# Optimization experiments

Hardware: AMD Instinct MI355X
Metric: run time of the kernel (lower is better)

The kernel has to match this reference:

```python
import jax, jax.numpy as jnp
import numpy as np

B, C, H, W = 8, 64, 64, 64
CI = 32  # inter_channels = in_channels // 2
EPS = 1e-5


def conv1x1(x, w, b=None):
    # x: (b,c,h,w), w: (o,c) -> (b,o,h,w)
    y = jnp.einsum('bchw,oc->bohw', x, w)
    if b is not None:
        y = y + b[None, :, None, None]
    return y


def maxpool2x2(x):
    b, c, h, w = x.shape
    return x.reshape(b, c, h // 2, 2, w // 2, 2).max(axis=(3, 5))


def setup_inputs() -> dict:
    key = jax.random.key(0)
    ks = jax.random.split(key, 12)
    s = 0.05
    return {
        'x': jax.random.normal(ks[0], (B, C, H, W), jnp.float32),
        'theta_w': jax.random.normal(ks[1], (CI, C), jnp.float32) * s,
        'theta_b': jax.random.normal(ks[2], (CI,), jnp.float32) * s,
        'phi_w': jax.random.normal(ks[3], (CI, C), jnp.float32) * s,
        'phi_b': jax.random.normal(ks[4], (CI,), jnp.float32) * s,
        'psi_w': jax.random.normal(ks[5], (CI, C), jnp.float32) * s,
        'psi_b': jax.random.normal(ks[6], (CI,), jnp.float32) * s,
        'cp_w': jax.random.normal(ks[7], (2 * CI,), jnp.float32) * s,  # concat_project 1x1, no bias
        'W_w': jax.random.normal(ks[8], (C, CI + 1), jnp.float32) * s,
        'W_b': jax.random.normal(ks[9], (C,), jnp.float32) * s,
        'bn_gamma': jax.random.normal(ks[10], (C,), jnp.float32) * s + 1.0,
        'bn_beta': jax.random.normal(ks[11], (C,), jnp.float32) * s,
    }


def reference(x, theta_w, theta_b, phi_w, phi_b, psi_w, psi_b, cp_w, W_w, W_b, bn_gamma, bn_beta):
    b = x.shape[0]
    # psi / phi branches get 2x2 maxpool (sub_sample=True default)
    psi_x = maxpool2x2(conv1x1(x, psi_w, psi_b)).reshape(b, CI, -1)      # (b,ci,M)
    psi_x = psi_x.transpose(0, 2, 1)                                     # (b,M,ci)
    theta_x = conv1x1(x, theta_w, theta_b).reshape(b, CI, -1)            # (b,ci,N)
    phi_x = maxpool2x2(conv1x1(x, phi_w, phi_b)).reshape(b, CI, -1)      # (b,ci,M)
    # concat_project(cat[theta_i, phi_j]) + ReLU == relu(w1.theta_i + w2.phi_j)
    w1, w2 = cp_w[:CI], cp_w[CI:]
    a = jnp.einsum('bcn,c->bn', theta_x, w1)                             # (b,N)
    bb = jnp.einsum('bcm,c->bm', phi_x, w2)                              # (b,M)
    f = jax.nn.relu(a[:, :, None] + bb[:, None, :])                      # (b,N,M)
    M = f.shape[-1]
    f_div_C = f / float(M)
    y = jnp.matmul(f_div_C, psi_x)                                       # (b,N,ci)
    y = y.transpose(0, 2, 1).reshape(b, CI, H, W)
    # r_structure_type='zero' -> zero structure channel
    structure_feat = jnp.zeros((b, 1, H, W), y.dtype)
    y = jnp.concatenate([y, structure_feat], axis=1)                     # (b,ci+1,H,W)
    wy = conv1x1(y, W_w, W_b)                                            # (b,C,H,W)
    # BatchNorm2d, training-mode batch stats, biased variance
    mu = wy.mean(axis=(0, 2, 3), keepdims=True)
    var = wy.var(axis=(0, 2, 3), keepdims=True)
    wy = (wy - mu) * jax.lax.rsqrt(var + EPS)
    wy = wy * bn_gamma[None, :, None, None] + bn_beta[None, :, None, None]
    return wy + x
```

## Files before the change

### kernel.cpp

```cpp
#include <hip/hip_runtime.h>

#define OFF_A    0
#define OFF_BB   32768
#define OFF_SBB  40960
#define OFF_PERM 49152
#define OFF_U    57344
#define OFF_T1   581632
#define OFF_T2   1106432
#define OFF_KK   1631232
#define OFF_MP1  1664000
#define OFF_MP2  1664512
#define OFF_HC   1665024
#define OFF_HS   1673224
#define OFF_HS2  1681424
#define OFF_BAR  1689624

__device__ __forceinline__ void stg(float* p, float v) {
    __hip_atomic_store(p, v, __ATOMIC_RELAXED, __HIP_MEMORY_SCOPE_AGENT);
}
__device__ __forceinline__ float ldg1(const float* p) {
    return __hip_atomic_load(p, __ATOMIC_RELAXED, __HIP_MEMORY_SCOPE_AGENT);
}
__device__ __forceinline__ void stgi(int* p, int v) {
    __hip_atomic_store(p, v, __ATOMIC_RELAXED, __HIP_MEMORY_SCOPE_AGENT);
}
__device__ __forceinline__ int ldgi(const int* p) {
    return __hip_atomic_load(p, __ATOMIC_RELAXED, __HIP_MEMORY_SCOPE_AGENT);
}
__device__ __forceinline__ void stgu(unsigned* p, unsigned v) {
    __hip_atomic_store(p, v, __ATOMIC_RELAXED, __HIP_MEMORY_SCOPE_AGENT);
}
__device__ __forceinline__ unsigned ldgu(const unsigned* p) {
    return __hip_atomic_load(p, __ATOMIC_RELAXED, __HIP_MEMORY_SCOPE_AGENT);
}

__device__ __forceinline__ void gbarBatch(float* ws, int b, unsigned goal)
{
    __syncthreads();
    if (threadIdx.x == 0) {
        unsigned* ctr = (unsigned*)(ws + OFF_BAR) + ((b + 1) << 5);
        __hip_atomic_fetch_add(ctr, 1u, __ATOMIC_RELAXED,
                               __HIP_MEMORY_SCOPE_AGENT);
        while (ldgu(ctr) < goal) __builtin_amdgcn_s_sleep(2);
    }
    __syncthreads();
}

__global__ __launch_bounds__(1024) void kMega(
    const float* __restrict__ x, const float* __restrict__ theta_w,
    const float* __restrict__ theta_b, const float* __restrict__ phi_w,
    const float* __restrict__ phi_b, const float* __restrict__ psi_w,
    const float* __restrict__ psi_b, const float* __restrict__ cp_w,
    const float* __restrict__ Ww, const float* __restrict__ Wb,
    const float* __restrict__ gamma, const float* __restrict__ beta,
    float* __restrict__ ws, float* __restrict__ out)
{
    __shared__ float sh[8640];
    const int tid = threadIdx.x;
    const int bid = blockIdx.x;
    const int b   = bid >> 5;
    const int sub = bid & 31;
    unsigned* bars = (unsigned*)(ws + OFF_BAR);

    {
        if (bid == 0 && tid == 0) {
            for (int i = 0; i < 9; ++i) stgu(&bars[i << 5], 0u);
        }
        if (tid < 97) {
            int e = sub*97 + tid;
            if (e < 1025)      stg(&ws[OFF_HC  + b*1025 + e], 0.0f);
            else if (e < 2050) stg(&ws[OFF_HS  + b*1025 + e - 1025], 0.0f);
            else if (e < 3075) stg(&ws[OFF_HS2 + b*1025 + e - 2050], 0.0f);
        }
        float* sm   = sh;
        float* sth  = sh + 4160;
        float* spsi = sh + 4228;
        float* sWw  = sh + 5284;
        for (int e = tid; e < 2048; e += 1024) {
            int i = e >> 6, c = e & 63;
            sm[i*130 + 2*c]     = phi_w[e];
            sm[i*130 + 2*c + 1] = psi_w[e];
        }
        for (int e = tid; e < 2048; e += 1024)
            sWw[(e >> 5)*33 + (e & 31)] = Ww[(e >> 5)*33 + (e & 31)];
        if (tid < 64) {
            float s = 0;
            for (int i = 0; i < 32; ++i) s += cp_w[i]*theta_w[i*64 + tid];
            sth[tid] = s;
        } else if (tid == 64) {
            float s = 0;
            for (int i = 0; i < 32; ++i) s += cp_w[i]*theta_b[i];
            sth[64] = s;
        }
        __syncthreads();
        if (bid == 0 && tid == 0) {
            stgu(&bars[288], 0x5A5A5A5Au);
            stgu(&bars[289], 0xA5A5A5A5u);
        }
        int i = tid & 31;
        int mIdx = tid >> 5;
        int m = (sub << 5) + mIdx;
        int ph = m >> 5, pw = m & 31;
        const float* xb = x + b*262144 + ph*128 + pw*2;
        const float2* wrow = (const float2*)(sm + i*130);
        float tb = sth[64];
        float p0=0,p1=0,p2=0,p3=0,s0=0,s1=0,s2=0,s3=0;
        float a0=tb,a1=tb,a2=tb,a3=tb;
        #pragma unroll 8
        for (int c = 0; c < 64; ++c) {
            float2 xa = *(const float2*)(xb + c*4096);
            float2 xc = *(const float2*)(xb + c*4096 + 64);
            float2 w  = wrow[c];
            float st  = sth[c];
            p0 += xa.x*w.x; p1 += xa.y*w.x; p2 += xc.x*w.x; p3 += xc.y*w.x;
            s0 += xa.x*w.y; s1 += xa.y*w.y; s2 += xc.x*w.y; s3 += xc.y*w.y;
            a0 += xa.x*st;  a1 += xa.y*st;  a2 += xc.x*st;  a3 += xc.y*st;
        }
        float pv = fmaxf(fmaxf(p0,p1), fmaxf(p2,p3)) + phi_b[i];
        float sv = fmaxf(fmaxf(s0,s1), fmaxf(s2,s3)) + psi_b[i];
        spsi[mIdx*33 + i] = sv;
        float v = pv * cp_w[32 + i];
        v += __shfl_xor(v, 16, 32);
        v += __shfl_xor(v,  8, 32);
        v += __shfl_xor(v,  4, 32);
        v += __shfl_xor(v,  2, 32);
        v += __shfl_xor(v,  1, 32);
        if (i == 0) {
            stg(&ws[OFF_BB + (b<<10) + m], v);
            int nb = (b<<12) + ph*128 + pw*2;
            stg(&ws[OFF_A + nb],      a0);
            stg(&ws[OFF_A + nb + 1],  a1);
            stg(&ws[OFF_A + nb + 64], a2);
            stg(&ws[OFF_A + nb + 65], a3);
        }
        __syncthreads();
        #pragma unroll
        for (int rep = 0; rep < 2; ++rep) {
            int idx = tid + (rep << 10);
            int ml = idx >> 6, o = idx & 63;
            const float* pr = &spsi[ml*33];
            const float* wr = &sWw[o*33];
            float u = 0;
            #pragma unroll
            for (int i2 = 0; i2 < 32; ++i2) u += pr[i2]*wr[i2];
            stg(&ws[OFF_U + (((b<<10) + (sub<<5) + ml) << 6) + o], u);
        }
    }
    __syncthreads();
    if (tid == 0) {
        while ((ldgu(&bars[288]) ^ ldgu(&bars[289])) != 0xFFFFFFFFu)
            __builtin_amdgcn_s_sleep(2);
        unsigned* ctr = bars + ((b + 1) << 5);
        __hip_atomic_fetch_add(ctr, 1u, __ATOMIC_RELAXED,
                               __HIP_MEMORY_SCOPE_AGENT);
        while (ldgu(ctr) < 32u) __builtin_amdgcn_s_sleep(2);
    }
    __syncthreads();

    {
        float* sb = sh;
        sb[tid] = ldg1(&ws[OFF_BB + (b<<10) + tid]);
        __syncthreads();
        {
            int ml = tid >> 5, jl = tid & 31;
            int m = (sub << 5) + ml;
            float vv = sb[m];
            int cnt = 0;
            for (int s = 0; s < 32; ++s) {
                int j = jl + (s << 5);
                float u = sb[j];
                cnt += (u > vv || (u == vv && j < m)) ? 1 : 0;
            }
            cnt += __shfl_xor(cnt,  1, 32);
            cnt += __shfl_xor(cnt,  2, 32);
            cnt += __shfl_xor(cnt,  4, 32);
            cnt += __shfl_xor(cnt,  8, 32);
            cnt += __shfl_xor(cnt, 16, 32);
            if (jl == 0) {
                stg(&ws[OFF_SBB + (b<<10) + cnt], vv);
                stgi(&((int*)ws)[OFF_PERM + (b<<10) + cnt], m);
            }
        }
        {
            int l = tid >> 3, jl = tid & 7;
            int n = (sub << 7) + l;
            float av = ldg1(&ws[OFF_A + (b<<12) + n]);
            float tt = -av;
            const float2* sb2 = (const float2*)sb;
            int cnt = 0;
            for (int s = 0; s < 64; ++s) {
                float2 u = sb2[jl + (s << 3)];
                cnt += (u.x > tt) ? 1 : 0;
                cnt += (u.y > tt) ? 1 : 0;
            }
            cnt += __shfl_xor(cnt, 1, 8);
            cnt += __shfl_xor(cnt, 2, 8);
            cnt += __shfl_xor(cnt, 4, 8);
            if (jl == 0) {
                stgi(&((int*)ws)[OFF_KK + (b<<12) + n], cnt);
                atomicAdd(&ws[OFF_HC + b*1025 + cnt], 1.0f);
                atomicAdd(&ws[OFF_HS + b*1025 + cnt], av);
                atomicAdd(&ws[OFF_HS2 + b*1025 + cnt], av*av);
            }
        }
    }
    gbarBatch(ws, b, 64u);

    {
        int obase = sub << 1;
        float* ssort = sh;
        int*   sperm = (int*)(sh + 1024);
        float* shc   = sh + 2048;
        float* shs   = sh + 3076;
        float* shs2  = sh + 4104;
        float* swp1  = sh + 5132;
        float* swp2  = sh + 5164;
        ssort[tid] = ldg1(&ws[OFF_SBB + (b<<10) + tid]);
        sperm[tid] = ldgi(&((const int*)ws)[OFF_PERM + (b<<10) + tid]);
        shc[tid]  = ldg1(&ws[OFF_HC  + b*1025 + tid]);
        shs[tid]  = ldg1(&ws[OFF_HS  + b*1025 + tid]);
        shs2[tid] = ldg1(&ws[OFF_HS2 + b*1025 + tid]);
        if (tid == 0) {
            shc[1024]  = ldg1(&ws[OFF_HC  + b*1025 + 1024]);
            shs[1024]  = ldg1(&ws[OFF_HS  + b*1025 + 1024]);
            shs2[1024] = ldg1(&ws[OFF_HS2 + b*1025 + 1024]);
        }
        __syncthreads();
        int ch = tid >> 1, o2 = tid & 1;
        int o  = obase + o2;
        int wv = tid >> 6, chl = (tid & 63) >> 1;
        const float* Ub = ws + OFF_U + (b<<16) + o;
        float p[2], sp[2];
        float s1 = 0, s2 = 0;
        #pragma unroll
        for (int jl = 0; jl < 2; ++jl) {
            int jj = (ch<<1) + jl;
            float v = ldg1(&Ub[sperm[jj]<<6]);
            p[jl] = v;
            sp[jl] = ssort[jj]*v;
            s1 += v; s2 += sp[jl];
        }
        float own1 = s1, own2 = s2;
        #pragma unroll
        for (int d = 1; d < 32; d <<= 1) {
            float u1 = __shfl_up(s1, d<<1, 64);
            float u2 = __shfl_up(s2, d<<1, 64);
            if (chl >= d) { s1 += u1; s2 += u2; }
        }
        if (chl == 31) { swp1[(wv<<1)+o2] = s1; swp2[(wv<<1)+o2] = s2; }
        __syncthreads();
        float off1 = 0, off2 = 0;
        for (int w = 0; w < 16; ++w) {
            if (w < wv) { off1 += swp1[(w<<1)+o2]; off2 += swp2[(w<<1)+o2]; }
        }
        float run1 = off1 + s1 - own1;
        float run2 = off2 + s2 - own2;
        float* T1 = ws + OFF_T1 + b*65600 + o;
        float* T2 = ws + OFF_T2 + b*65600 + o;
        if (ch == 0) { stg(&T1[0], 0.0f); stg(&T2[0], 0.0f); }
        const float inv = 1.0f/1024.0f;
        float m1 = 0, m2 = 0;
        #pragma unroll
        for (int jl = 0; jl < 2; ++jl) {
            int k = (ch<<1) + jl + 1;
            run1 += p[jl]; run2 += sp[jl];
            float t1 = run1*inv, t2 = run2*inv;
            stg(&T1[k<<6], t1);
            stg(&T2[k<<6], t2);
            float c = shc[k], sa_ = shs[k], sa2 = shs2[k];
            m1 += sa_*t1 + c*t2;
            m2 += (sa2*t1 + 2.0f*sa_*t2)*t1 + c*t2*t2;
        }
        m1 += __shfl_xor(m1,  2, 64); m2 += __shfl_xor(m2,  2, 64);
        m1 += __shfl_xor(m1,  4, 64); m2 += __shfl_xor(m2,  4, 64);
        m1 += __shfl_xor(m1,  8, 64); m2 += __shfl_xor(m2,  8, 64);
        m1 += __shfl_xor(m1, 16, 64); m2 += __shfl_xor(m2, 16, 64);
        m1 += __shfl_xor(m1, 32, 64); m2 += __shfl_xor(m2, 32, 64);
        __syncthreads();
        if (chl == 0) { swp1[(wv<<1)+o2] = m1; swp2[(wv<<1)+o2] = m2; }
        __syncthreads();
        if (tid < 2) {
            float a1 = 0, a2 = 0;
            for (int w = 0; w < 16; ++w) {
                a1 += swp1[(w<<1)+tid]; a2 += swp2[(w<<1)+tid];
            }
            stg(&ws[OFF_MP1 + (b<<6) + obase + tid], a1);
            stg(&ws[OFF_MP2 + (b<<6) + obase + tid], a2);
        }
    }
    __syncthreads();
    if (tid == 0) {
        unsigned* ctr = bars + ((b + 1) << 5);
        unsigned old = __hip_atomic_fetch_add(ctr, 1u, __ATOMIC_RELAXED,
                                              __HIP_MEMORY_SCOPE_AGENT);
        if (old == 95u)
            __hip_atomic_fetch_add(&bars[0], 1u, __ATOMIC_RELAXED,
                                   __HIP_MEMORY_SCOPE_AGENT);
        while (ldgu(ctr) < 96u) __builtin_amdgcn_s_sleep(2);
    }
    __syncthreads();

    {
        float* tile = sh;
        float* sa = sh + 8256;
        int*   sk = (int*)(sh + 8384);
        float* sA = sh + 8512;
        float* sD = sh + 8576;
        int n0 = sub << 7;
        if (tid < 128) {
            sa[tid] = ldg1(&ws[OFF_A + (b<<12) + n0 + tid]);
            sk[tid] = ldgi(&((const int*)ws)[OFF_KK + (b<<12) + n0 + tid]);
        }
        __syncthreads();
        const float* T1 = ws + OFF_T1 + b*65600;
        const float* T2 = ws + OFF_T2 + b*65600;
        {
            int o = tid & 63, ng = tid >> 6;
            #pragma unroll
            for (int j = 0; j < 8; ++j) {
                int n = (ng << 3) + j;
                int k = sk[n];
                float a = sa[n];
                tile[o*129 + n] = a*ldg1(&T1[(k<<6) + o])
                                  + ldg1(&T2[(k<<6) + o]);
            }
        }
        if (tid == 0) {
            while (ldgu(&bars[0]) < 8u) __builtin_amdgcn_s_sleep(2);
        }
        __syncthreads();
        if (tid < 64) {
            const float Ninv = 1.0f/32768.0f;
            float m1s = 0, m2s = 0;
            #pragma unroll
            for (int b3 = 0; b3 < 8; ++b3) {
                m1s += ldg1(&ws[OFF_MP1 + (b3<<6) + tid]);
                m2s += ldg1(&ws[OFF_MP2 + (b3<<6) + tid]);
            }
            float m1 = m1s * Ninv;
            float m2 = m2s * Ninv;
            float wb = Wb[tid];
            float mu  = m1 + wb;
            float E2  = m2 + 2.0f*wb*m1 + wb*wb;
            float var = E2 - mu*mu;
            float A = gamma[tid] * rsqrtf(var + 1e-5f);
            sA[tid] = A;
            sD[tid] = beta[tid] + A*(wb - mu);
        }
        __syncthreads();
        {
            int n = tid & 127, og2 = tid >> 7;
            #pragma unroll
            for (int j = 0; j < 8; ++j) {
                int o = (og2 << 3) + j;
                int idx = ((b<<6) + o)*4096 + n0 + n;
                out[idx] = sA[o]*tile[o*129 + n] + sD[o] + x[idx];
            }
        }
    }
}

extern "C" void kernel_launch(void* const* d_in, const int* in_sizes, int n_in,
                              void* d_out, int out_size, void* d_ws, size_t ws_size,
                              hipStream_t stream)
{
    const float* x       = (const float*)d_in[0];
    const float* theta_w = (const float*)d_in[1];
    const float* theta_b = (const float*)d_in[2];
    const float* phi_w   = (const float*)d_in[3];
    const float* phi_b   = (const float*)d_in[4];
    const float* psi_w   = (const float*)d_in[5];
    const float* psi_b   = (const float*)d_in[6];
    const float* cp_w    = (const float*)d_in[7];
    const float* Ww      = (const float*)d_in[8];
    const float* Wb      = (const float*)d_in[9];
    const float* gamma   = (const float*)d_in[10];
    const float* beta    = (const float*)d_in[11];
    float* ws  = (float*)d_ws;
    float* out = (float*)d_out;

    kMega<<<256, 1024, 0, stream>>>(x, theta_w, theta_b, phi_w, phi_b,
                                    psi_w, psi_b, cp_w, Ww, Wb,
                                    gamma, beta, ws, out);
}
```

Measured before the change: 132.3 us.

## Split megakernel at BN stats barrier and scatter sorted data via rank into LDS

Splits the persistent kernel in two. The final phase (BatchNorm stats reduction, table lookup and residual output) becomes a second launch, which removes the last batch barrier and the global spin on the cross-batch counter. The sort step now stores each element's rank instead of the sorted values and permutation. The next phase scatters bb and a transposed U layout into shared memory by rank, so it no longer does strided gathers of U from global memory. This costs an extra kernel launch, and the barrier initialisation now skips the global counter.

```diff
diff --git a/kernel.cpp b/kernel.cpp
--- a/kernel.cpp
+++ b/kernel.cpp
@@ -2,8 +2,7 @@
 
 #define OFF_A    0
 #define OFF_BB   32768
-#define OFF_SBB  40960
-#define OFF_PERM 49152
+#define OFF_RK   40960
 #define OFF_U    57344
 #define OFF_T1   581632
 #define OFF_T2   1106432
@@ -46,16 +45,14 @@
     __syncthreads();
 }
 
-__global__ __launch_bounds__(1024) void kMega(
+__global__ __launch_bounds__(1024) void kA(
     const float* __restrict__ x, const float* __restrict__ theta_w,
     const float* __restrict__ theta_b, const float* __restrict__ phi_w,
     const float* __restrict__ phi_b, const float* __restrict__ psi_w,
     const float* __restrict__ psi_b, const float* __restrict__ cp_w,
-    const float* __restrict__ Ww, const float* __restrict__ Wb,
-    const float* __restrict__ gamma, const float* __restrict__ beta,
-    float* __restrict__ ws, float* __restrict__ out)
+    const float* __restrict__ Ww, float* __restrict__ ws)
 {
-    __shared__ float sh[8640];
+    __shared__ float sh[7396];
     const int tid = threadIdx.x;
     const int bid = blockIdx.x;
     const int b   = bid >> 5;
@@ -64,7 +61,7 @@
 
     {
         if (bid == 0 && tid == 0) {
-            for (int i = 0; i < 9; ++i) stgu(&bars[i << 5], 0u);
+            for (int i = 0; i < 8; ++i) stgu(&bars[(i + 1) << 5], 0u);
         }
         if (tid < 97) {
             int e = sub*97 + tid;
@@ -136,14 +133,14 @@
         __syncthreads();
         #pragma unroll
         for (int rep = 0; rep < 2; ++rep) {
-            int idx = tid + (rep << 10);
-            int ml = idx >> 6, o = idx & 63;
+            int o  = (tid >> 5) + (rep << 5);
+            int ml = tid & 31;
             const float* pr = &spsi[ml*33];
             const float* wr = &sWw[o*33];
             float u = 0;
             #pragma unroll
             for (int i2 = 0; i2 < 32; ++i2) u += pr[i2]*wr[i2];
-            stg(&ws[OFF_U + (((b<<10) + (sub<<5) + ml) << 6) + o], u);
+            stg(&ws[OFF_U + (((b<<6) + o)<<10) + (sub<<5) + ml], u);
         }
     }
     __syncthreads();
@@ -176,10 +173,8 @@
             cnt += __shfl_xor(cnt,  4, 32);
             cnt += __shfl_xor(cnt,  8, 32);
             cnt += __shfl_xor(cnt, 16, 32);
-            if (jl == 0) {
-                stg(&ws[OFF_SBB + (b<<10) + cnt], vv);
-                stgi(&((int*)ws)[OFF_PERM + (b<<10) + cnt], m);
-            }
+            if (jl == 0)
+                stgi(&((int*)ws)[OFF_RK + (b<<10) + m], cnt);
         }
         {
             int l = tid >> 3, jl = tid & 7;
@@ -208,36 +203,44 @@
 
     {
         int obase = sub << 1;
-        float* ssort = sh;
-        int*   sperm = (int*)(sh + 1024);
-        float* shc   = sh + 2048;
-        float* shs   = sh + 3076;
-        float* shs2  = sh + 4104;
-        float* swp1  = sh + 5132;
-        float* swp2  = sh + 5164;
-        ssort[tid] = ldg1(&ws[OFF_SBB + (b<<10) + tid]);
-        sperm[tid] = ldgi(&((const int*)ws)[OFF_PERM + (b<<10) + tid]);
-        shc[tid]  = ldg1(&ws[OFF_HC  + b*1025 + tid]);
-        shs[tid]  = ldg1(&ws[OFF_HS  + b*1025 + tid]);
-        shs2[tid] = ldg1(&ws[OFF_HS2 + b*1025 + tid]);
-        if (tid == 0) {
-            shc[1024]  = ldg1(&ws[OFF_HC  + b*1025 + 1024]);
-            shs[1024]  = ldg1(&ws[OFF_HS  + b*1025 + 1024]);
-            shs2[1024] = ldg1(&ws[OFF_HS2 + b*1025 + 1024]);
+        float* ssb  = sh;
+        float* sU0  = sh + 1024;
+        float* sU1  = sh + 2048;
+        float* shc  = sh + 3072;
+        float* shs  = sh + 4097;
+        float* shs2 = sh + 5122;
+        float* swp1 = sh + 6148;
+        float* swp2 = sh + 6180;
+        {
+            float bbv = ldg1(&ws[OFF_BB + (b<<10) + tid]);
+            int   rk  = ldgi(&((const int*)ws)[OFF_RK + (b<<10) + tid]);
+            float u0  = ldg1(&ws[OFF_U + (((b<<6) + obase)<<10) + tid]);
+            float u1  = ldg1(&ws[OFF_U + (((b<<6) + obase + 1)<<10) + tid]);
+            ssb[rk] = bbv;
+            sU0[rk] = u0;
+            sU1[rk] = u1;
+            shc[tid]  = ldg1(&ws[OFF_HC  + b*1025 + tid]);
+            shs[tid]  = ldg1(&ws[OFF_HS  + b*1025 + tid]);
+            shs2[tid] = ldg1(&ws[OFF_HS2 + b*1025 + tid]);
+            if (tid == 0) {
+                shc[1024]  = ldg1(&ws[OFF_HC  + b*1025 + 1024]);
+                shs[1024]  = ldg1(&ws[OFF_HS  + b*1025 + 1024]);
+                shs2[1024] = ldg1(&ws[OFF_HS2 + b*1025 + 1024]);
+            }
         }
         __syncthreads();
         int ch = tid >> 1, o2 = tid & 1;
         int o  = obase + o2;
         int wv = tid >> 6, chl = (tid & 63) >> 1;
-        const float* Ub = ws + OFF_U + (b<<16) + o;
+        const float* sU = sh + 1024 + (o2 << 10);
         float p[2], sp[2];
         float s1 = 0, s2 = 0;
         #pragma unroll
         for (int jl = 0; jl < 2; ++jl) {
             int jj = (ch<<1) + jl;
-            float v = ldg1(&Ub[sperm[jj]<<6]);
+            float v = sU[jj];
             p[jl] = v;
-            sp[jl] = ssort[jj]*v;
+            sp[jl] = ssb[jj]*v;
             s1 += v; s2 += sp[jl];
         }
         float own1 = s1, own2 = s2;
@@ -288,74 +291,67 @@
             stg(&ws[OFF_MP2 + (b<<6) + obase + tid], a2);
         }
     }
-    __syncthreads();
-    if (tid == 0) {
-        unsigned* ctr = bars + ((b + 1) << 5);
-        unsigned old = __hip_atomic_fetch_add(ctr, 1u, __ATOMIC_RELAXED,
-                                              __HIP_MEMORY_SCOPE_AGENT);
-        if (old == 95u)
-            __hip_atomic_fetch_add(&bars[0], 1u, __ATOMIC_RELAXED,
-                                   __HIP_MEMORY_SCOPE_AGENT);
-        while (ldgu(ctr) < 96u) __builtin_amdgcn_s_sleep(2);
-    }
-    __syncthreads();
-
-    {
-        float* tile = sh;
-        float* sa = sh + 8256;
-        int*   sk = (int*)(sh + 8384);
-        float* sA = sh + 8512;
-        float* sD = sh + 8576;
-        int n0 = sub << 7;
-        if (tid < 128) {
-            sa[tid] = ldg1(&ws[OFF_A + (b<<12) + n0 + tid]);
-            sk[tid] = ldgi(&((const int*)ws)[OFF_KK + (b<<12) + n0 + tid]);
-        }
-        __syncthreads();
-        const float* T1 = ws + OFF_T1 + b*65600;
-        const float* T2 = ws + OFF_T2 + b*65600;
-        {
-            int o = tid & 63, ng = tid >> 6;
-            #pragma unroll
-            for (int j = 0; j < 8; ++j) {
-                int n = (ng << 3) + j;
-                int k = sk[n];
-                float a = sa[n];
-                tile[o*129 + n] = a*ldg1(&T1[(k<<6) + o])
-                                  + ldg1(&T2[(k<<6) + o]);
-            }
-        }
-        if (tid == 0) {
-            while (ldgu(&bars[0]) < 8u) __builtin_amdgcn_s_sleep(2);
-        }
-        __syncthreads();
-        if (tid < 64) {
-            const float Ninv = 1.0f/32768.0f;
-            float m1s = 0, m2s = 0;
-            #pragma unroll
-            for (int b3 = 0; b3 < 8; ++b3) {
-                m1s += ldg1(&ws[OFF_MP1 + (b3<<6) + tid]);
-                m2s += ldg1(&ws[OFF_MP2 + (b3<<6) + tid]);
-            }
-            float m1 = m1s * Ninv;
-            float m2 = m2s * Ninv;
-            float wb = Wb[tid];
-            float mu  = m1 + wb;
-            float E2  = m2 + 2.0f*wb*m1 + wb*wb;
-            float var = E2 - mu*mu;
-            float A = gamma[tid] * rsqrtf(var + 1e-5f);
-            sA[tid] = A;
-            sD[tid] = beta[tid] + A*(wb - mu);
-        }
-        __syncthreads();
-        {
-            int n = tid & 127, og2 = tid >> 7;
-            #pragma unroll
-            for (int j = 0; j < 8; ++j) {
-                int o = (og2 << 3) + j;
-                int idx = ((b<<6) + o)*4096 + n0 + n;
-                out[idx] = sA[o]*tile[o*129 + n] + sD[o] + x[idx];
-            }
+}
+
+__global__ __launch_bounds__(1024) void kB(
+    const float* __restrict__ x, const float* __restrict__ Wb,
+    const float* __restrict__ gamma, const float* __restrict__ beta,
+    const float* __restrict__ ws, float* __restrict__ out)
+{
+    __shared__ float tile[64*129];
+    __shared__ float sa[128];
+    __shared__ int   sk[128];
+    __shared__ float sA[64];
+    __shared__ float sD[64];
+    const int tid = threadIdx.x;
+    const int b   = blockIdx.x >> 5;
+    const int n0  = (blockIdx.x & 31) << 7;
+    if (tid < 128) {
+        sa[tid] = ws[OFF_A + (b<<12) + n0 + tid];
+        sk[tid] = ((const int*)ws)[OFF_KK + (b<<12) + n0 + tid];
+    }
+    if (tid < 64) {
+        const float Ninv = 1.0f/32768.0f;
+        float m1s = 0, m2s = 0;
+        #pragma unroll
+        for (int b3 = 0; b3 < 8; ++b3) {
+            m1s += ws[OFF_MP1 + (b3<<6) + tid];
+            m2s += ws[OFF_MP2 + (b3<<6) + tid];
+        }
+        float m1 = m1s * Ninv;
+        float m2 = m2s * Ninv;
+        float wb = Wb[tid];
+        float mu  = m1 + wb;
+        float E2  = m2 + 2.0f*wb*m1 + wb*wb;
+        float var = E2 - mu*mu;
+        float A = gamma[tid] * rsqrtf(var + 1e-5f);
+        sA[tid] = A;
+        sD[tid] = beta[tid] + A*(wb - mu);
+    }
+    __syncthreads();
+    const float* T1 = ws + OFF_T1 + b*65600;
+    const float* T2 = ws + OFF_T2 + b*65600;
+    {
+        int o = tid & 63, ng = tid >> 6;
+        float Ao = sA[o], Do = sD[o];
+        #pragma unroll
+        for (int j = 0; j < 8; ++j) {
+            int n = (ng << 3) + j;
+            int k = sk[n];
+            float a = sa[n];
+            float t1 = T1[(k<<6) + o];
+            float t2 = T2[(k<<6) + o];
+            tile[o*129 + n] = Ao*(a*t1 + t2) + Do;
+        }
+    }
+    __syncthreads();
+    {
+        int n = tid & 127, og = tid >> 7;
+        #pragma unroll
+        for (int j = 0; j < 8; ++j) {
+            int o = (og << 3) + j;
+            int idx = ((b<<6) + o)*4096 + n0 + n;
+            out[idx] = tile[o*129 + n] + x[idx];
         }
     }
 }
@@ -379,7 +375,7 @@
     float* ws  = (float*)d_ws;
     float* out = (float*)d_out;
 
-    kMega<<<256, 1024, 0, stream>>>(x, theta_w, theta_b, phi_w, phi_b,
-                                    psi_w, psi_b, cp_w, Ww, Wb,
-                                    gamma, beta, ws, out);
-}
+    kA<<<256, 1024, 0, stream>>>(x, theta_w, theta_b, phi_w, phi_b,
+                                 psi_w, psi_b, cp_w, Ww, ws);
+    kB<<<256, 1024, 0, stream>>>(x, Wb, gamma, beta, ws, out);
+}
```

New measurement: 126.2 us. 4.6% less time.
